# Kernel tuning notes

Measured on AMD Instinct MI355X. Metric: run time of the kernel, lower is better.

The kernel has to match this reference:

```python
import jax, jax.numpy as jnp
import numpy as np

N = 16384   # flat token count
D = 256     # d_model
M = 64      # median_size (attention in_features / hidden_features)
OUT = 1     # output_size


def setup_inputs() -> dict:
    key = jax.random.key(0)
    ks = jax.random.split(key, 12)
    sD = 1.0 / np.sqrt(D)
    sM = 1.0 / np.sqrt(M)
    rn = lambda k, shape, s: (jax.random.normal(k, shape, jnp.float32) * s)
    return {
        "x":    rn(ks[0], (N, D), 1.0),
        "W1":   rn(ks[1], (D, M), sD), "b1": jnp.zeros((M,), jnp.float32),
        # 3 stacked attention blocks
        "Wq":   rn(ks[2], (3, M, M), sM), "bq": jnp.zeros((3, M), jnp.float32),
        "Wk":   rn(ks[3], (3, M, M), sM), "bk": jnp.zeros((3, M), jnp.float32),
        "Wv":   rn(ks[4], (3, M, M), sM), "bv": jnp.zeros((3, M), jnp.float32),
        "Wf1":  rn(ks[5], (3, M, M), sM), "bf1": jnp.zeros((3, M), jnp.float32),
        "Wf2":  rn(ks[6], (3, M, M), sM), "bf2": jnp.zeros((3, M), jnp.float32),
        "ln_g": jnp.ones((3, M), jnp.float32), "ln_b": jnp.zeros((3, M), jnp.float32),
        "Wout": rn(ks[7], (M, OUT), sM), "bout": jnp.zeros((OUT,), jnp.float32),
    }


def leaky(x, slope):
    return jnp.where(x >= 0, x, slope * x)


def layer_norm(x, g, b, eps=1e-5):
    mu = jnp.mean(x, axis=-1, keepdims=True)
    var = jnp.mean((x - mu) ** 2, axis=-1, keepdims=True)
    return (x - mu) * jax.lax.rsqrt(var + eps) * g + b


def attn_block(x, Wq, bq, Wk, bk, Wv, bv, Wf1, bf1, Wf2, bf2):
    # per-token outer-product attention: attn[n] = softmax(q[n] k[n]^T) over last dim
    q = x @ Wq + bq            # [N, M]
    k = x @ Wk + bk
    v = x @ Wv + bv
    a = jax.nn.softmax(q[:, :, None] * k[:, None, :], axis=-1)   # [N, M, M]
    y = jnp.einsum('nij,nj->ni', a, v) + x                       # residual add (x += x0)
    h = leaky(y @ Wf1 + bf1, 0.01)                               # LeakyReLU(0.01)
    h = h @ Wf2 + bf2
    return h + y                                                 # pred=False residual


def reference(x, W1, b1, Wq, bq, Wk, bk, Wv, bv, Wf1, bf1, Wf2, bf2, ln_g, ln_b, Wout, bout):
    h = x @ W1 + b1                 # Linear_1
    res = leaky(h, 0.1)             # x1 = LeakyReLU(0.1)(h)
    cur = h                         # transformer_1 is applied to pre-activation h
    for t in range(3):
        a = attn_block(cur, Wq[t], bq[t], Wk[t], bk[t], Wv[t], bv[t],
                       Wf1[t], bf1[t], Wf2[t], bf2[t])
        a = layer_norm(a, ln_g[t], ln_b[t])
        res = a + res               # x2 = LN(...) + x1, etc.
        cur = res
    out = leaky(res @ Wout + bout, 0.1).reshape(-1, OUT)
    return (out, out, out, out, out)
```

## Files before the change

kernel.cpp:

```cpp
#include <hip/hip_runtime.h>

#define NTOK 16384
#define TB 16

typedef float f32x4_t __attribute__((ext_vector_type(4)));
typedef short s16x8_t __attribute__((ext_vector_type(8)));

union bfpack { unsigned int u[4]; s16x8_t v; };

__device__ __forceinline__ unsigned int pk2bf(float lo, float hi) {
    unsigned int r;
    asm("v_cvt_pk_bf16_f32 %0, %1, %2" : "=v"(r) : "v"(lo), "v"(hi));
    return r;
}
__device__ __forceinline__ unsigned short f2bf(float f) {
    unsigned int r;
    asm("v_cvt_pk_bf16_f32 %0, %1, %1" : "=v"(r) : "v"(f));
    return (unsigned short)r;
}
__device__ __forceinline__ unsigned short f2bf_host_style(float f) {
    unsigned int x = __float_as_uint(f);
    x += 0x7fffu + ((x >> 16) & 1u);
    return (unsigned short)(x >> 16);
}
__device__ __forceinline__ float fexp2(float x) {
#if __has_builtin(__builtin_amdgcn_exp2f)
    return __builtin_amdgcn_exp2f(x);
#else
    return exp2f(x);
#endif
}
__device__ __forceinline__ float frcp(float x) {
#if __has_builtin(__builtin_amdgcn_rcpf)
    return __builtin_amdgcn_rcpf(x);
#else
    return 1.0f / x;
#endif
}
__device__ __forceinline__ float frsq(float x) {
#if __has_builtin(__builtin_amdgcn_rsqf)
    return __builtin_amdgcn_rsqf(x);
#else
    return rsqrtf(x);
#endif
}

__global__ __launch_bounds__(256)
void prep_kernel(const float* __restrict__ W1,
                 const float* __restrict__ Wq, const float* __restrict__ Wk,
                 const float* __restrict__ Wv, const float* __restrict__ Wf1,
                 const float* __restrict__ Wf2, unsigned short* __restrict__ wsb)
{
    const int i = blockIdx.x * 256 + threadIdx.x;
    if (i < 16384) {
        const int m = i >> 8, k = i & 255;
        wsb[i] = f2bf_host_style(W1[k * 64 + m]);
    } else if (i < 77824) {
        const int u  = i - 16384;
        const int mi = u >> 12;
        const int st = mi / 5, q = mi % 5;
        const int r  = u & 4095;
        const int hk = r >> 11;
        const int r1 = r & 2047;
        const int w  = r1 >> 9;
        const int r2 = r1 & 511;
        const int l  = r2 >> 3;
        const int e  = r2 & 7;
        const int m  = w * 16 + (l & 15);
        const int k  = hk * 32 + (l >> 4) * 8 + e;
        const float* src = q == 0 ? Wq : q == 1 ? Wk : q == 2 ? Wv : q == 3 ? Wf1 : Wf2;
        wsb[i] = f2bf_host_style(src[st * 4096 + k * 64 + m]);
    }
}

__global__ __launch_bounds__(256, 4)
void tf3_kernel(const float* __restrict__ x,
                const float* __restrict__ b1,
                const float* __restrict__ bq, const float* __restrict__ bk,
                const float* __restrict__ bv,
                const float* __restrict__ bf1, const float* __restrict__ bf2,
                const float* __restrict__ lng, const float* __restrict__ lnb,
                const float* __restrict__ Wout, const float* __restrict__ bout,
                const unsigned short* __restrict__ wsb,
                float* __restrict__ out)
{
    __shared__ __align__(16) char smem[15104];
    unsigned short* a_lds = (unsigned short*)smem;
    float* q_lds  = (float*)(smem + 2048);
    float* ky_lds = (float*)(smem + 6400);
    float* v_lds  = (float*)(smem + 10752);
    char*  x_img  = smem + 2048;

    const int tid = threadIdx.x;
    const int wv  = tid >> 6;
    const int l   = tid & 63;
    const int n0  = blockIdx.x * TB;

    const int lr  = l & 15;
    const int q4  = l >> 4;
    const int c   = wv * 16 + lr;

    const int ge = lr;
    const int tg = wv * 4 + q4;

    float res_reg[4], cur_reg[4];

    auto LOADM = [&](int mat, s16x8_t& r0, s16x8_t& r1) {
        const char* gb = (const char*)(wsb + 16384 + mat * 4096) + wv * 1024 + l * 16;
        r0 = *reinterpret_cast<const s16x8_t*>(gb);
        r1 = *reinterpret_cast<const s16x8_t*>(gb + 4096);
    };
    auto mmd = [&](s16x8_t af0, s16x8_t af1, s16x8_t b0, s16x8_t b1) -> f32x4_t {
        f32x4_t acc = __builtin_amdgcn_mfma_f32_16x16x32_bf16(af0, b0, (f32x4_t){0.f,0.f,0.f,0.f}, 0, 0, 0);
        acc = __builtin_amdgcn_mfma_f32_16x16x32_bf16(af1, b1, acc, 0, 0, 0);
        return acc;
    };

    s16x8_t bq0, bq1, bk0, bk1, bv0, bv1;
    s16x8_t f10, f11, f20, f21;

    LOADM(0, bq0, bq1); LOADM(1, bk0, bk1); LOADM(2, bv0, bv1);

    {
        const int r  = tid & 15;
        const int cb = tid >> 4;
        const float* xp = x + (size_t)(n0 + r) * 256 + cb * 16;
        const float4 u0 = *reinterpret_cast<const float4*>(xp);
        const float4 u1 = *reinterpret_cast<const float4*>(xp + 4);
        const float4 u2 = *reinterpret_cast<const float4*>(xp + 8);
        const float4 u3 = *reinterpret_cast<const float4*>(xp + 12);
        bfpack P0, P1;
        P0.u[0] = pk2bf(u0.x, u0.y); P0.u[1] = pk2bf(u0.z, u0.w);
        P0.u[2] = pk2bf(u1.x, u1.y); P0.u[3] = pk2bf(u1.z, u1.w);
        P1.u[0] = pk2bf(u2.x, u2.y); P1.u[1] = pk2bf(u2.z, u2.w);
        P1.u[2] = pk2bf(u3.x, u3.y); P1.u[3] = pk2bf(u3.z, u3.w);
        char* rowb = x_img + r * 512;
        *reinterpret_cast<s16x8_t*>(rowb + (((cb * 2    ) ^ (r & 7)) << 4)) = P0.v;
        *reinterpret_cast<s16x8_t*>(rowb + (((cb * 2 + 1) ^ (r & 7)) << 4)) = P1.v;
    }
    __syncthreads();

    f32x4_t acch = {0.f, 0.f, 0.f, 0.f};
    #pragma unroll
    for (int s5 = 0; s5 < 8; ++s5) {
        const s16x8_t af = *reinterpret_cast<const s16x8_t*>(
            x_img + lr * 512 + (((s5 * 4 + q4) ^ (lr & 7)) << 4));
        const s16x8_t bf = *reinterpret_cast<const s16x8_t*>(&wsb[c * 256 + s5 * 32 + q4 * 8]);
        acch = __builtin_amdgcn_mfma_f32_16x16x32_bf16(af, bf, acch, 0, 0, 0);
    }
    __syncthreads();
    {
        const float bb = b1[c];
        #pragma unroll
        for (int rg = 0; rg < 4; ++rg)
            q_lds[(q4 * 4 + rg) * 68 + c] = acch[rg] + bb;
    }
    __syncthreads();
    #pragma unroll
    for (int tt = 0; tt < 4; ++tt) {
        const int t = wv * 4 + tt;
        const float h = q_lds[t * 68 + l];
        cur_reg[tt] = h;
        res_reg[tt] = h >= 0.f ? h : 0.1f * h;
        a_lds[t * 64 + (((l >> 3) ^ (t & 7)) * 8) + (l & 7)] = f2bf(h);
    }

    for (int st = 0; st < 3; ++st) {
        const float bqv  = bq[st * 64 + c];
        const float bkv  = bk[st * 64 + c];
        const float bvv  = bv[st * 64 + c];
        const float bf1v = bf1[st * 64 + c];
        const float bf2v = bf2[st * 64 + c];
        const float lngv = lng[st * 64 + l];
        const float lnbv = lnb[st * 64 + l];

        __syncthreads();
        {
            const s16x8_t af0 = *reinterpret_cast<const s16x8_t*>(&a_lds[lr * 64 + ((q4       ^ (lr & 7)) * 8)]);
            const s16x8_t af1 = *reinterpret_cast<const s16x8_t*>(&a_lds[lr * 64 + (((4 + q4) ^ (lr & 7)) * 8)]);
            f32x4_t aq = mmd(af0, af1, bq0, bq1);
            f32x4_t ak = mmd(af0, af1, bk0, bk1);
            f32x4_t av = mmd(af0, af1, bv0, bv1);
            #pragma unroll
            for (int rg = 0; rg < 4; ++rg) {
                const int tr = q4 * 4 + rg;
                q_lds[tr * 68 + c]  = aq[rg] + bqv;
                ky_lds[tr * 68 + c] = ak[rg] + bkv;
                v_lds[tr * 68 + c]  = av[rg] + bvv;
            }
        }
        LOADM(st * 5 + 3, f10, f11);
        __syncthreads();

        float kmax_t[4], kmin_t[4];
        {
            const float4 kv = *reinterpret_cast<const float4*>(&ky_lds[tg * 68 + ge * 4]);
            float kmx = fmaxf(fmaxf(kv.x, kv.y), fmaxf(kv.z, kv.w));
            float kmn = fminf(fminf(kv.x, kv.y), fminf(kv.z, kv.w));
            #pragma unroll
            for (int m = 1; m < 16; m <<= 1) {
                kmx = fmaxf(kmx, __shfl_xor(kmx, m, 64));
                kmn = fminf(kmn, __shfl_xor(kmn, m, 64));
            }
            #pragma unroll
            for (int tt = 0; tt < 4; ++tt) {
                kmax_t[tt] = __shfl(kmx, tt * 16, 64);
                kmin_t[tt] = __shfl(kmn, tt * 16, 64);
            }
        }
        #pragma unroll
        for (int tt = 0; tt < 4; ++tt) {
            const int t = wv * 4 + tt;
            const float qs = q_lds[t * 68 + l] * 1.44269504088896340736f;
            const float m2 = fmaxf(qs * kmax_t[tt], qs * kmin_t[tt]);
            const float* kb = &ky_lds[t * 68];
            const float* vb = &v_lds[t * 68];
            float4 ka0 = *reinterpret_cast<const float4*>(kb);
            float4 ka1 = *reinterpret_cast<const float4*>(kb + 4);
            float4 va0 = *reinterpret_cast<const float4*>(vb);
            float4 va1 = *reinterpret_cast<const float4*>(vb + 4);
            float s0 = 0.f, s1 = 0.f, p0 = 0.f, p1 = 0.f;
            #pragma unroll
            for (int j = 0; j < 64; j += 8) {
                float4 kn0, kn1, vn0, vn1;
                if (j < 56) {
                    kn0 = *reinterpret_cast<const float4*>(kb + j + 8);
                    kn1 = *reinterpret_cast<const float4*>(kb + j + 12);
                    vn0 = *reinterpret_cast<const float4*>(vb + j + 8);
                    vn1 = *reinterpret_cast<const float4*>(vb + j + 12);
                }
                const float e0 = fexp2(fmaf(qs, ka0.x, -m2)); s0 += e0; p0 = fmaf(e0, va0.x, p0);
                const float e1 = fexp2(fmaf(qs, ka0.y, -m2)); s1 += e1; p1 = fmaf(e1, va0.y, p1);
                const float e2 = fexp2(fmaf(qs, ka0.z, -m2)); s0 += e2; p0 = fmaf(e2, va0.z, p0);
                const float e3 = fexp2(fmaf(qs, ka0.w, -m2)); s1 += e3; p1 = fmaf(e3, va0.w, p1);
                const float e4 = fexp2(fmaf(qs, ka1.x, -m2)); s0 += e4; p0 = fmaf(e4, va1.x, p0);
                const float e5 = fexp2(fmaf(qs, ka1.y, -m2)); s1 += e5; p1 = fmaf(e5, va1.y, p1);
                const float e6 = fexp2(fmaf(qs, ka1.z, -m2)); s0 += e6; p0 = fmaf(e6, va1.z, p0);
                const float e7 = fexp2(fmaf(qs, ka1.w, -m2)); s1 += e7; p1 = fmaf(e7, va1.w, p1);
                ka0 = kn0; ka1 = kn1; va0 = vn0; va1 = vn1;
            }
            const float y = (p0 + p1) * frcp(s0 + s1) + cur_reg[tt];
            ky_lds[t * 68 + l] = y;
        }
        LOADM(st * 5 + 4, f20, f21);
        __syncthreads();

        {
            f32x4_t acc = {0.f, 0.f, 0.f, 0.f};
            #pragma unroll
            for (int kh = 0; kh < 2; ++kh) {
                const float* yp = &ky_lds[lr * 68 + kh * 32 + q4 * 8];
                const float4 y0 = *reinterpret_cast<const float4*>(yp);
                const float4 y1 = *reinterpret_cast<const float4*>(yp + 4);
                bfpack P;
                P.u[0] = pk2bf(y0.x, y0.y); P.u[1] = pk2bf(y0.z, y0.w);
                P.u[2] = pk2bf(y1.x, y1.y); P.u[3] = pk2bf(y1.z, y1.w);
                acc = __builtin_amdgcn_mfma_f32_16x16x32_bf16(P.v, kh ? f11 : f10, acc, 0, 0, 0);
            }
            #pragma unroll
            for (int rg = 0; rg < 4; ++rg) {
                const int tr = q4 * 4 + rg;
                float h = acc[rg] + bf1v;
                h = h >= 0.f ? h : 0.01f * h;
                a_lds[tr * 64 + (((c >> 3) ^ (tr & 7)) * 8) + (c & 7)] = f2bf(h);
            }
        }
        if (st < 2) {
            LOADM((st + 1) * 5 + 0, bq0, bq1);
            LOADM((st + 1) * 5 + 1, bk0, bk1);
        }
        __syncthreads();

        {
            const s16x8_t ag0 = *reinterpret_cast<const s16x8_t*>(&a_lds[lr * 64 + ((q4       ^ (lr & 7)) * 8)]);
            const s16x8_t ag1 = *reinterpret_cast<const s16x8_t*>(&a_lds[lr * 64 + (((4 + q4) ^ (lr & 7)) * 8)]);
            f32x4_t acc = mmd(ag0, ag1, f20, f21);
            #pragma unroll
            for (int rg = 0; rg < 4; ++rg) {
                const int tr = q4 * 4 + rg;
                ky_lds[tr * 68 + c] += acc[rg] + bf2v;
            }
        }
        if (st < 2) LOADM((st + 1) * 5 + 2, bv0, bv1);
        __syncthreads();

        {
            const float4 av4 = *reinterpret_cast<const float4*>(&ky_lds[tg * 68 + ge * 4]);
            float ssum = av4.x + av4.y + av4.z + av4.w;
            #pragma unroll
            for (int m = 1; m < 16; m <<= 1) ssum += __shfl_xor(ssum, m, 64);
            const float mug = ssum * 0.015625f;
            const float d0 = av4.x - mug, d1 = av4.y - mug, d2 = av4.z - mug, d3 = av4.w - mug;
            float vsum = d0 * d0 + d1 * d1 + d2 * d2 + d3 * d3;
            #pragma unroll
            for (int m = 1; m < 16; m <<= 1) vsum += __shfl_xor(vsum, m, 64);
            #pragma unroll
            for (int tt = 0; tt < 4; ++tt) {
                const int t = wv * 4 + tt;
                const float mu = __shfl(mug, tt * 16, 64);
                const float vv = __shfl(vsum, tt * 16, 64);
                const float rs = frsq(vv * 0.015625f + 1e-5f);
                const float a  = ky_lds[t * 68 + l];
                const float an = (a - mu) * rs * lngv + lnbv;
                const float rnew = res_reg[tt] + an;
                res_reg[tt] = rnew;
                cur_reg[tt] = rnew;
                a_lds[t * 64 + (((l >> 3) ^ (t & 7)) * 8) + (l & 7)] = f2bf(rnew);
            }
        }
    }

    const float wo = Wout[l];
    const float bo = bout[0];
    #pragma unroll
    for (int tt = 0; tt < 4; ++tt)
        q_lds[(wv * 4 + tt) * 68 + l] = res_reg[tt] * wo;
    {
        const float4 pv = *reinterpret_cast<const float4*>(&q_lds[tg * 68 + ge * 4]);
        float p = pv.x + pv.y + pv.z + pv.w;
        #pragma unroll
        for (int m = 1; m < 16; m <<= 1) p += __shfl_xor(p, m, 64);
        if (ge == 0) {
            float o = p + bo;
            o = o >= 0.f ? o : 0.1f * o;
            #pragma unroll
            for (int c5 = 0; c5 < 5; ++c5)
                out[(size_t)c5 * NTOK + n0 + tg] = o;
        }
    }
}

extern "C" void kernel_launch(void* const* d_in, const int* in_sizes, int n_in,
                              void* d_out, int out_size, void* d_ws, size_t ws_size,
                              hipStream_t stream) {
    const float* x    = (const float*)d_in[0];
    const float* W1   = (const float*)d_in[1];
    const float* b1   = (const float*)d_in[2];
    const float* Wq   = (const float*)d_in[3];
    const float* bq   = (const float*)d_in[4];
    const float* Wk   = (const float*)d_in[5];
    const float* bk   = (const float*)d_in[6];
    const float* Wv   = (const float*)d_in[7];
    const float* bv   = (const float*)d_in[8];
    const float* Wf1  = (const float*)d_in[9];
    const float* bf1  = (const float*)d_in[10];
    const float* Wf2  = (const float*)d_in[11];
    const float* bf2  = (const float*)d_in[12];
    const float* lngp = (const float*)d_in[13];
    const float* lnbp = (const float*)d_in[14];
    const float* Wout = (const float*)d_in[15];
    const float* bout = (const float*)d_in[16];
    float* outp = (float*)d_out;
    unsigned short* wsb = (unsigned short*)d_ws;

    hipLaunchKernelGGL(prep_kernel, dim3(304), dim3(256), 0, stream,
                       W1, Wq, Wk, Wv, Wf1, Wf2, wsb);
    hipLaunchKernelGGL(tf3_kernel, dim3(NTOK / TB), dim3(256), 0, stream,
                       x, b1, bq, bk, bv, bf1, bf2, lngp, lnbp, Wout, bout,
                       (const unsigned short*)wsb, outp);
}
```

Measured before the change: 54.54 us.

## Make each wave own four tokens independently and drop block-wide barriers

Each wavefront now processes its own 4 tokens end to end, with a private LDS region, so all __syncthreads barriers between GEMM, softmax and layernorm stages go away. Every GEMM now computes all 64 output columns per wave as four MFMA tiles, with only 4 of the 16 A rows meaningful. That wastes three quarters of the MFMA work, and weights are reloaded from global or L2 on every use instead of being held in registers. The softmax inner loop also loses its software prefetch.

```diff
diff --git a/kernel.cpp b/kernel.cpp
--- a/kernel.cpp
+++ b/kernel.cpp
@@ -1,7 +1,6 @@
 #include <hip/hip_runtime.h>
 
 #define NTOK 16384
-#define TB 16
 
 typedef float f32x4_t __attribute__((ext_vector_type(4)));
 typedef short s16x8_t __attribute__((ext_vector_type(8)));
@@ -84,117 +83,131 @@
                 const unsigned short* __restrict__ wsb,
                 float* __restrict__ out)
 {
-    __shared__ __align__(16) char smem[15104];
-    unsigned short* a_lds = (unsigned short*)smem;
-    float* q_lds  = (float*)(smem + 2048);
-    float* ky_lds = (float*)(smem + 6400);
-    float* v_lds  = (float*)(smem + 10752);
-    char*  x_img  = smem + 2048;
+    __shared__ __align__(16) char smem[4 * 3840];
 
     const int tid = threadIdx.x;
     const int wv  = tid >> 6;
     const int l   = tid & 63;
-    const int n0  = blockIdx.x * TB;
-
     const int lr  = l & 15;
     const int q4  = l >> 4;
-    const int c   = wv * 16 + lr;
-
-    const int ge = lr;
-    const int tg = wv * 4 + q4;
+    const int tw0 = blockIdx.x * 16 + wv * 4;
+
+    char* wbase = smem + wv * 3840;
+    unsigned short* a_w = (unsigned short*)wbase;
+    float* q_w  = (float*)(wbase + 576);
+    float* ky_w = (float*)(wbase + 1664);
+    float* v_w  = (float*)(wbase + 2752);
+    char*  x_img = wbase + 576;
 
     float res_reg[4], cur_reg[4];
 
-    auto LOADM = [&](int mat, s16x8_t& r0, s16x8_t& r1) {
-        const char* gb = (const char*)(wsb + 16384 + mat * 4096) + wv * 1024 + l * 16;
-        r0 = *reinterpret_cast<const s16x8_t*>(gb);
-        r1 = *reinterpret_cast<const s16x8_t*>(gb + 4096);
+    auto LDB4 = [&](int mat, int kh, s16x8_t b[4]) {
+        const char* gb = (const char*)(wsb + 16384) + mat * 8192 + kh * 4096 + l * 16;
+        b[0] = *reinterpret_cast<const s16x8_t*>(gb);
+        b[1] = *reinterpret_cast<const s16x8_t*>(gb + 1024);
+        b[2] = *reinterpret_cast<const s16x8_t*>(gb + 2048);
+        b[3] = *reinterpret_cast<const s16x8_t*>(gb + 3072);
     };
-    auto mmd = [&](s16x8_t af0, s16x8_t af1, s16x8_t b0, s16x8_t b1) -> f32x4_t {
-        f32x4_t acc = __builtin_amdgcn_mfma_f32_16x16x32_bf16(af0, b0, (f32x4_t){0.f,0.f,0.f,0.f}, 0, 0, 0);
-        acc = __builtin_amdgcn_mfma_f32_16x16x32_bf16(af1, b1, acc, 0, 0, 0);
-        return acc;
+    auto GEMM_A = [&](int mat, f32x4_t acc[4]) {
+        #pragma unroll
+        for (int kh = 0; kh < 2; ++kh) {
+            const s16x8_t af = *reinterpret_cast<const s16x8_t*>(
+                (char*)a_w + (lr & 3) * 144 + (kh * 4 + q4) * 16);
+            s16x8_t b[4];
+            LDB4(mat, kh, b);
+            #pragma unroll
+            for (int tile = 0; tile < 4; ++tile)
+                acc[tile] = __builtin_amdgcn_mfma_f32_16x16x32_bf16(af, b[tile], acc[tile], 0, 0, 0);
+        }
     };
 
-    s16x8_t bq0, bq1, bk0, bk1, bv0, bv1;
-    s16x8_t f10, f11, f20, f21;
-
-    LOADM(0, bq0, bq1); LOADM(1, bk0, bk1); LOADM(2, bv0, bv1);
-
     {
-        const int r  = tid & 15;
-        const int cb = tid >> 4;
-        const float* xp = x + (size_t)(n0 + r) * 256 + cb * 16;
-        const float4 u0 = *reinterpret_cast<const float4*>(xp);
-        const float4 u1 = *reinterpret_cast<const float4*>(xp + 4);
-        const float4 u2 = *reinterpret_cast<const float4*>(xp + 8);
-        const float4 u3 = *reinterpret_cast<const float4*>(xp + 12);
-        bfpack P0, P1;
-        P0.u[0] = pk2bf(u0.x, u0.y); P0.u[1] = pk2bf(u0.z, u0.w);
-        P0.u[2] = pk2bf(u1.x, u1.y); P0.u[3] = pk2bf(u1.z, u1.w);
-        P1.u[0] = pk2bf(u2.x, u2.y); P1.u[1] = pk2bf(u2.z, u2.w);
-        P1.u[2] = pk2bf(u3.x, u3.y); P1.u[3] = pk2bf(u3.z, u3.w);
-        char* rowb = x_img + r * 512;
-        *reinterpret_cast<s16x8_t*>(rowb + (((cb * 2    ) ^ (r & 7)) << 4)) = P0.v;
-        *reinterpret_cast<s16x8_t*>(rowb + (((cb * 2 + 1) ^ (r & 7)) << 4)) = P1.v;
-    }
-    __syncthreads();
-
-    f32x4_t acch = {0.f, 0.f, 0.f, 0.f};
-    #pragma unroll
-    for (int s5 = 0; s5 < 8; ++s5) {
-        const s16x8_t af = *reinterpret_cast<const s16x8_t*>(
-            x_img + lr * 512 + (((s5 * 4 + q4) ^ (lr & 7)) << 4));
-        const s16x8_t bf = *reinterpret_cast<const s16x8_t*>(&wsb[c * 256 + s5 * 32 + q4 * 8]);
-        acch = __builtin_amdgcn_mfma_f32_16x16x32_bf16(af, bf, acch, 0, 0, 0);
-    }
-    __syncthreads();
+        const int xr = l >> 4, xc = l & 15;
+        const float* xrow = x + (size_t)(tw0 + xr) * 256;
+        #pragma unroll
+        for (int i = 0; i < 4; ++i) {
+            const float4 u = *reinterpret_cast<const float4*>(xrow + xc * 4 + i * 64);
+            uint2 p;
+            p.x = pk2bf(u.x, u.y);
+            p.y = pk2bf(u.z, u.w);
+            *reinterpret_cast<uint2*>(x_img + xr * 528 + xc * 8 + i * 128) = p;
+        }
+    }
     {
-        const float bb = b1[c];
-        #pragma unroll
-        for (int rg = 0; rg < 4; ++rg)
-            q_lds[(q4 * 4 + rg) * 68 + c] = acch[rg] + bb;
-    }
-    __syncthreads();
+        f32x4_t acc[4] = {{0,0,0,0},{0,0,0,0},{0,0,0,0},{0,0,0,0}};
+        #pragma unroll
+        for (int s5 = 0; s5 < 8; ++s5) {
+            const s16x8_t af = *reinterpret_cast<const s16x8_t*>(
+                x_img + (lr & 3) * 528 + s5 * 64 + q4 * 16);
+            #pragma unroll
+            for (int tile = 0; tile < 4; ++tile) {
+                const s16x8_t bf = *reinterpret_cast<const s16x8_t*>(
+                    (const char*)wsb + (size_t)(tile * 16 + lr) * 512 + s5 * 64 + q4 * 16);
+                acc[tile] = __builtin_amdgcn_mfma_f32_16x16x32_bf16(af, bf, acc[tile], 0, 0, 0);
+            }
+        }
+        if (q4 == 0) {
+            #pragma unroll
+            for (int tile = 0; tile < 4; ++tile) {
+                const float bb = b1[tile * 16 + lr];
+                #pragma unroll
+                for (int rg = 0; rg < 4; ++rg)
+                    q_w[rg * 68 + tile * 16 + lr] = acc[tile][rg] + bb;
+            }
+        }
+    }
     #pragma unroll
     for (int tt = 0; tt < 4; ++tt) {
-        const int t = wv * 4 + tt;
-        const float h = q_lds[t * 68 + l];
+        const float h = q_w[tt * 68 + l];
         cur_reg[tt] = h;
         res_reg[tt] = h >= 0.f ? h : 0.1f * h;
-        a_lds[t * 64 + (((l >> 3) ^ (t & 7)) * 8) + (l & 7)] = f2bf(h);
+        a_w[tt * 72 + l] = f2bf(h);
     }
 
     for (int st = 0; st < 3; ++st) {
-        const float bqv  = bq[st * 64 + c];
-        const float bkv  = bk[st * 64 + c];
-        const float bvv  = bv[st * 64 + c];
-        const float bf1v = bf1[st * 64 + c];
-        const float bf2v = bf2[st * 64 + c];
-        const float lngv = lng[st * 64 + l];
-        const float lnbv = lnb[st * 64 + l];
-
-        __syncthreads();
-        {
-            const s16x8_t af0 = *reinterpret_cast<const s16x8_t*>(&a_lds[lr * 64 + ((q4       ^ (lr & 7)) * 8)]);
-            const s16x8_t af1 = *reinterpret_cast<const s16x8_t*>(&a_lds[lr * 64 + (((4 + q4) ^ (lr & 7)) * 8)]);
-            f32x4_t aq = mmd(af0, af1, bq0, bq1);
-            f32x4_t ak = mmd(af0, af1, bk0, bk1);
-            f32x4_t av = mmd(af0, af1, bv0, bv1);
-            #pragma unroll
-            for (int rg = 0; rg < 4; ++rg) {
-                const int tr = q4 * 4 + rg;
-                q_lds[tr * 68 + c]  = aq[rg] + bqv;
-                ky_lds[tr * 68 + c] = ak[rg] + bkv;
-                v_lds[tr * 68 + c]  = av[rg] + bvv;
-            }
-        }
-        LOADM(st * 5 + 3, f10, f11);
-        __syncthreads();
+        {
+            f32x4_t aq[4] = {{0,0,0,0},{0,0,0,0},{0,0,0,0},{0,0,0,0}};
+            GEMM_A(st * 5 + 0, aq);
+            if (q4 == 0) {
+                #pragma unroll
+                for (int tile = 0; tile < 4; ++tile) {
+                    const float bb = bq[st * 64 + tile * 16 + lr];
+                    #pragma unroll
+                    for (int rg = 0; rg < 4; ++rg)
+                        q_w[rg * 68 + tile * 16 + lr] = aq[tile][rg] + bb;
+                }
+            }
+        }
+        {
+            f32x4_t ak[4] = {{0,0,0,0},{0,0,0,0},{0,0,0,0},{0,0,0,0}};
+            GEMM_A(st * 5 + 1, ak);
+            if (q4 == 0) {
+                #pragma unroll
+                for (int tile = 0; tile < 4; ++tile) {
+                    const float bb = bk[st * 64 + tile * 16 + lr];
+                    #pragma unroll
+                    for (int rg = 0; rg < 4; ++rg)
+                        ky_w[rg * 68 + tile * 16 + lr] = ak[tile][rg] + bb;
+                }
+            }
+        }
+        {
+            f32x4_t av[4] = {{0,0,0,0},{0,0,0,0},{0,0,0,0},{0,0,0,0}};
+            GEMM_A(st * 5 + 2, av);
+            if (q4 == 0) {
+                #pragma unroll
+                for (int tile = 0; tile < 4; ++tile) {
+                    const float bb = bv[st * 64 + tile * 16 + lr];
+                    #pragma unroll
+                    for (int rg = 0; rg < 4; ++rg)
+                        v_w[rg * 68 + tile * 16 + lr] = av[tile][rg] + bb;
+                }
+            }
+        }
 
         float kmax_t[4], kmin_t[4];
         {
-            const float4 kv = *reinterpret_cast<const float4*>(&ky_lds[tg * 68 + ge * 4]);
+            const float4 kv = *reinterpret_cast<const float4*>(ky_w + q4 * 68 + lr * 4);
             float kmx = fmaxf(fmaxf(kv.x, kv.y), fmaxf(kv.z, kv.w));
             float kmn = fminf(fminf(kv.x, kv.y), fminf(kv.z, kv.w));
             #pragma unroll
@@ -210,82 +223,70 @@
         }
         #pragma unroll
         for (int tt = 0; tt < 4; ++tt) {
-            const int t = wv * 4 + tt;
-            const float qs = q_lds[t * 68 + l] * 1.44269504088896340736f;
+            const float qs = q_w[tt * 68 + l] * 1.44269504088896340736f;
             const float m2 = fmaxf(qs * kmax_t[tt], qs * kmin_t[tt]);
-            const float* kb = &ky_lds[t * 68];
-            const float* vb = &v_lds[t * 68];
-            float4 ka0 = *reinterpret_cast<const float4*>(kb);
-            float4 ka1 = *reinterpret_cast<const float4*>(kb + 4);
-            float4 va0 = *reinterpret_cast<const float4*>(vb);
-            float4 va1 = *reinterpret_cast<const float4*>(vb + 4);
+            const float* kb = ky_w + tt * 68;
+            const float* vb = v_w + tt * 68;
             float s0 = 0.f, s1 = 0.f, p0 = 0.f, p1 = 0.f;
             #pragma unroll
-            for (int j = 0; j < 64; j += 8) {
-                float4 kn0, kn1, vn0, vn1;
-                if (j < 56) {
-                    kn0 = *reinterpret_cast<const float4*>(kb + j + 8);
-                    kn1 = *reinterpret_cast<const float4*>(kb + j + 12);
-                    vn0 = *reinterpret_cast<const float4*>(vb + j + 8);
-                    vn1 = *reinterpret_cast<const float4*>(vb + j + 12);
-                }
-                const float e0 = fexp2(fmaf(qs, ka0.x, -m2)); s0 += e0; p0 = fmaf(e0, va0.x, p0);
-                const float e1 = fexp2(fmaf(qs, ka0.y, -m2)); s1 += e1; p1 = fmaf(e1, va0.y, p1);
-                const float e2 = fexp2(fmaf(qs, ka0.z, -m2)); s0 += e2; p0 = fmaf(e2, va0.z, p0);
-                const float e3 = fexp2(fmaf(qs, ka0.w, -m2)); s1 += e3; p1 = fmaf(e3, va0.w, p1);
-                const float e4 = fexp2(fmaf(qs, ka1.x, -m2)); s0 += e4; p0 = fmaf(e4, va1.x, p0);
-                const float e5 = fexp2(fmaf(qs, ka1.y, -m2)); s1 += e5; p1 = fmaf(e5, va1.y, p1);
-                const float e6 = fexp2(fmaf(qs, ka1.z, -m2)); s0 += e6; p0 = fmaf(e6, va1.z, p0);
-                const float e7 = fexp2(fmaf(qs, ka1.w, -m2)); s1 += e7; p1 = fmaf(e7, va1.w, p1);
-                ka0 = kn0; ka1 = kn1; va0 = vn0; va1 = vn1;
+            for (int j = 0; j < 64; j += 4) {
+                const float4 kj = *reinterpret_cast<const float4*>(kb + j);
+                const float4 vj = *reinterpret_cast<const float4*>(vb + j);
+                const float e0 = fexp2(fmaf(qs, kj.x, -m2)); s0 += e0; p0 = fmaf(e0, vj.x, p0);
+                const float e1 = fexp2(fmaf(qs, kj.y, -m2)); s1 += e1; p1 = fmaf(e1, vj.y, p1);
+                const float e2 = fexp2(fmaf(qs, kj.z, -m2)); s0 += e2; p0 = fmaf(e2, vj.z, p0);
+                const float e3 = fexp2(fmaf(qs, kj.w, -m2)); s1 += e3; p1 = fmaf(e3, vj.w, p1);
             }
             const float y = (p0 + p1) * frcp(s0 + s1) + cur_reg[tt];
-            ky_lds[t * 68 + l] = y;
-        }
-        LOADM(st * 5 + 4, f20, f21);
-        __syncthreads();
-
-        {
-            f32x4_t acc = {0.f, 0.f, 0.f, 0.f};
+            ky_w[tt * 68 + l] = y;
+        }
+
+        {
+            f32x4_t acc[4] = {{0,0,0,0},{0,0,0,0},{0,0,0,0},{0,0,0,0}};
             #pragma unroll
             for (int kh = 0; kh < 2; ++kh) {
-                const float* yp = &ky_lds[lr * 68 + kh * 32 + q4 * 8];
+                const float* yp = ky_w + (lr & 3) * 68 + kh * 32 + q4 * 8;
                 const float4 y0 = *reinterpret_cast<const float4*>(yp);
                 const float4 y1 = *reinterpret_cast<const float4*>(yp + 4);
                 bfpack P;
                 P.u[0] = pk2bf(y0.x, y0.y); P.u[1] = pk2bf(y0.z, y0.w);
                 P.u[2] = pk2bf(y1.x, y1.y); P.u[3] = pk2bf(y1.z, y1.w);
-                acc = __builtin_amdgcn_mfma_f32_16x16x32_bf16(P.v, kh ? f11 : f10, acc, 0, 0, 0);
-            }
-            #pragma unroll
-            for (int rg = 0; rg < 4; ++rg) {
-                const int tr = q4 * 4 + rg;
-                float h = acc[rg] + bf1v;
-                h = h >= 0.f ? h : 0.01f * h;
-                a_lds[tr * 64 + (((c >> 3) ^ (tr & 7)) * 8) + (c & 7)] = f2bf(h);
-            }
-        }
-        if (st < 2) {
-            LOADM((st + 1) * 5 + 0, bq0, bq1);
-            LOADM((st + 1) * 5 + 1, bk0, bk1);
-        }
-        __syncthreads();
-
-        {
-            const s16x8_t ag0 = *reinterpret_cast<const s16x8_t*>(&a_lds[lr * 64 + ((q4       ^ (lr & 7)) * 8)]);
-            const s16x8_t ag1 = *reinterpret_cast<const s16x8_t*>(&a_lds[lr * 64 + (((4 + q4) ^ (lr & 7)) * 8)]);
-            f32x4_t acc = mmd(ag0, ag1, f20, f21);
-            #pragma unroll
-            for (int rg = 0; rg < 4; ++rg) {
-                const int tr = q4 * 4 + rg;
-                ky_lds[tr * 68 + c] += acc[rg] + bf2v;
-            }
-        }
-        if (st < 2) LOADM((st + 1) * 5 + 2, bv0, bv1);
-        __syncthreads();
-
-        {
-            const float4 av4 = *reinterpret_cast<const float4*>(&ky_lds[tg * 68 + ge * 4]);
+                s16x8_t b[4];
+                LDB4(st * 5 + 3, kh, b);
+                #pragma unroll
+                for (int tile = 0; tile < 4; ++tile)
+                    acc[tile] = __builtin_amdgcn_mfma_f32_16x16x32_bf16(P.v, b[tile], acc[tile], 0, 0, 0);
+            }
+            if (q4 == 0) {
+                #pragma unroll
+                for (int tile = 0; tile < 4; ++tile) {
+                    const float bb = bf1[st * 64 + tile * 16 + lr];
+                    #pragma unroll
+                    for (int rg = 0; rg < 4; ++rg) {
+                        float h = acc[tile][rg] + bb;
+                        h = h >= 0.f ? h : 0.01f * h;
+                        a_w[rg * 72 + tile * 16 + lr] = f2bf(h);
+                    }
+                }
+            }
+        }
+
+        {
+            f32x4_t acc[4] = {{0,0,0,0},{0,0,0,0},{0,0,0,0},{0,0,0,0}};
+            GEMM_A(st * 5 + 4, acc);
+            if (q4 == 0) {
+                #pragma unroll
+                for (int tile = 0; tile < 4; ++tile) {
+                    const float bb = bf2[st * 64 + tile * 16 + lr];
+                    #pragma unroll
+                    for (int rg = 0; rg < 4; ++rg)
+                        ky_w[rg * 68 + tile * 16 + lr] += acc[tile][rg] + bb;
+                }
+            }
+        }
+
+        {
+            const float4 av4 = *reinterpret_cast<const float4*>(ky_w + q4 * 68 + lr * 4);
             float ssum = av4.x + av4.y + av4.z + av4.w;
             #pragma unroll
             for (int m = 1; m < 16; m <<= 1) ssum += __shfl_xor(ssum, m, 64);
@@ -294,38 +295,40 @@
             float vsum = d0 * d0 + d1 * d1 + d2 * d2 + d3 * d3;
             #pragma unroll
             for (int m = 1; m < 16; m <<= 1) vsum += __shfl_xor(vsum, m, 64);
+            const float lngv = lng[st * 64 + l];
+            const float lnbv = lnb[st * 64 + l];
             #pragma unroll
             for (int tt = 0; tt < 4; ++tt) {
-                const int t = wv * 4 + tt;
                 const float mu = __shfl(mug, tt * 16, 64);
                 const float vv = __shfl(vsum, tt * 16, 64);
                 const float rs = frsq(vv * 0.015625f + 1e-5f);
-                const float a  = ky_lds[t * 68 + l];
+                const float a  = ky_w[tt * 68 + l];
                 const float an = (a - mu) * rs * lngv + lnbv;
                 const float rnew = res_reg[tt] + an;
                 res_reg[tt] = rnew;
                 cur_reg[tt] = rnew;
-                a_lds[t * 64 + (((l >> 3) ^ (t & 7)) * 8) + (l & 7)] = f2bf(rnew);
-            }
-        }
-    }
-
-    const float wo = Wout[l];
-    const float bo = bout[0];
-    #pragma unroll
-    for (int tt = 0; tt < 4; ++tt)
-        q_lds[(wv * 4 + tt) * 68 + l] = res_reg[tt] * wo;
+                a_w[tt * 72 + l] = f2bf(rnew);
+            }
+        }
+    }
+
     {
-        const float4 pv = *reinterpret_cast<const float4*>(&q_lds[tg * 68 + ge * 4]);
+        const float wo = Wout[l];
+        const float bo = bout[0];
+        #pragma unroll
+        for (int tt = 0; tt < 4; ++tt)
+            q_w[tt * 68 + l] = res_reg[tt] * wo;
+        const float4 pv = *reinterpret_cast<const float4*>(q_w + q4 * 68 + lr * 4);
         float p = pv.x + pv.y + pv.z + pv.w;
         #pragma unroll
         for (int m = 1; m < 16; m <<= 1) p += __shfl_xor(p, m, 64);
-        if (ge == 0) {
+        if (lr == 0) {
             float o = p + bo;
             o = o >= 0.f ? o : 0.1f * o;
+            const int token = tw0 + q4;
             #pragma unroll
             for (int c5 = 0; c5 < 5; ++c5)
-                out[(size_t)c5 * NTOK + n0 + tg] = o;
+                out[(size_t)c5 * NTOK + token] = o;
         }
     }
 }
@@ -355,7 +358,7 @@
 
     hipLaunchKernelGGL(prep_kernel, dim3(304), dim3(256), 0, stream,
                        W1, Wq, Wk, Wv, Wf1, Wf2, wsb);
-    hipLaunchKernelGGL(tf3_kernel, dim3(NTOK / TB), dim3(256), 0, stream,
+    hipLaunchKernelGGL(tf3_kernel, dim3(NTOK / 16), dim3(256), 0, stream,
                        x, b1, bq, bk, bv, bf1, bf2, lngp, lnbp, Wout, bout,
                        (const unsigned short*)wsb, outp);
 }
```

Measured after the change: 69.28 us. 27.0% more time.

## Halve tokens per block to 8 with two waves covering 32 columns each

Applied to the files above, without the earlier changes.

The token tile drops from 16 to 8 and the block from four waves to two. Each wave now produces 32 output columns using paired 16x16 MFMAs, which doubles the number of blocks and raises the per-wave MFMA count. The MFMA tiles still span 16 rows, so half of each tile's rows hold stale LDS data and the total matrix work effectively doubles. Weight prefetches are also regrouped: the next stage's q/k/v fragments now load together after the FFN instead of being spread across the stage, and the softmax inner loop loses its explicit software prefetch.

```diff
diff --git a/kernel.cpp b/kernel.cpp
--- a/kernel.cpp
+++ b/kernel.cpp
@@ -1,7 +1,7 @@
 #include <hip/hip_runtime.h>
 
 #define NTOK 16384
-#define TB 16
+#define TB 8
 
 typedef float f32x4_t __attribute__((ext_vector_type(4)));
 typedef short s16x8_t __attribute__((ext_vector_type(8)));
@@ -73,7 +73,7 @@
     }
 }
 
-__global__ __launch_bounds__(256, 4)
+__global__ __launch_bounds__(128, 4)
 void tf3_kernel(const float* __restrict__ x,
                 const float* __restrict__ b1,
                 const float* __restrict__ bq, const float* __restrict__ bk,
@@ -98,32 +98,32 @@
 
     const int lr  = l & 15;
     const int q4  = l >> 4;
-    const int c   = wv * 16 + lr;
-
-    const int ge = lr;
-    const int tg = wv * 4 + q4;
+    const int c0  = wv * 32 + lr;
+    const int c1  = c0 + 16;
 
     float res_reg[4], cur_reg[4];
 
-    auto LOADM = [&](int mat, s16x8_t& r0, s16x8_t& r1) {
-        const char* gb = (const char*)(wsb + 16384 + mat * 4096) + wv * 1024 + l * 16;
-        r0 = *reinterpret_cast<const s16x8_t*>(gb);
-        r1 = *reinterpret_cast<const s16x8_t*>(gb + 4096);
+    auto LOADM2 = [&](int mat, s16x8_t& a00, s16x8_t& a01, s16x8_t& a10, s16x8_t& a11) {
+        const char* gb = (const char*)(wsb + 16384) + mat * 8192 + (wv * 2) * 1024 + l * 16;
+        a00 = *reinterpret_cast<const s16x8_t*>(gb);
+        a10 = *reinterpret_cast<const s16x8_t*>(gb + 1024);
+        a01 = *reinterpret_cast<const s16x8_t*>(gb + 4096);
+        a11 = *reinterpret_cast<const s16x8_t*>(gb + 4096 + 1024);
     };
-    auto mmd = [&](s16x8_t af0, s16x8_t af1, s16x8_t b0, s16x8_t b1) -> f32x4_t {
-        f32x4_t acc = __builtin_amdgcn_mfma_f32_16x16x32_bf16(af0, b0, (f32x4_t){0.f,0.f,0.f,0.f}, 0, 0, 0);
-        acc = __builtin_amdgcn_mfma_f32_16x16x32_bf16(af1, b1, acc, 0, 0, 0);
-        return acc;
-    };
-
-    s16x8_t bq0, bq1, bk0, bk1, bv0, bv1;
-    s16x8_t f10, f11, f20, f21;
-
-    LOADM(0, bq0, bq1); LOADM(1, bk0, bk1); LOADM(2, bv0, bv1);
+
+    s16x8_t bq00, bq01, bq10, bq11;
+    s16x8_t bk00, bk01, bk10, bk11;
+    s16x8_t bv00, bv01, bv10, bv11;
+    s16x8_t f100, f101, f110, f111;
+    s16x8_t f200, f201, f210, f211;
+
+    LOADM2(0, bq00, bq01, bq10, bq11);
+    LOADM2(1, bk00, bk01, bk10, bk11);
+    LOADM2(2, bv00, bv01, bv10, bv11);
 
     {
-        const int r  = tid & 15;
-        const int cb = tid >> 4;
+        const int r  = tid >> 4;
+        const int cb = tid & 15;
         const float* xp = x + (size_t)(n0 + r) * 256 + cb * 16;
         const float4 u0 = *reinterpret_cast<const float4*>(xp);
         const float4 u1 = *reinterpret_cast<const float4*>(xp + 4);
@@ -140,20 +140,27 @@
     }
     __syncthreads();
 
-    f32x4_t acch = {0.f, 0.f, 0.f, 0.f};
+    f32x4_t acch0 = {0.f, 0.f, 0.f, 0.f};
+    f32x4_t acch1 = {0.f, 0.f, 0.f, 0.f};
     #pragma unroll
     for (int s5 = 0; s5 < 8; ++s5) {
         const s16x8_t af = *reinterpret_cast<const s16x8_t*>(
             x_img + lr * 512 + (((s5 * 4 + q4) ^ (lr & 7)) << 4));
-        const s16x8_t bf = *reinterpret_cast<const s16x8_t*>(&wsb[c * 256 + s5 * 32 + q4 * 8]);
-        acch = __builtin_amdgcn_mfma_f32_16x16x32_bf16(af, bf, acch, 0, 0, 0);
+        const s16x8_t bf0 = *reinterpret_cast<const s16x8_t*>(&wsb[c0 * 256 + s5 * 32 + q4 * 8]);
+        const s16x8_t bf1f = *reinterpret_cast<const s16x8_t*>(&wsb[c1 * 256 + s5 * 32 + q4 * 8]);
+        acch0 = __builtin_amdgcn_mfma_f32_16x16x32_bf16(af, bf0, acch0, 0, 0, 0);
+        acch1 = __builtin_amdgcn_mfma_f32_16x16x32_bf16(af, bf1f, acch1, 0, 0, 0);
     }
     __syncthreads();
     {
-        const float bb = b1[c];
+        const float bb0 = b1[c0];
+        const float bb1 = b1[c1];
         #pragma unroll
-        for (int rg = 0; rg < 4; ++rg)
-            q_lds[(q4 * 4 + rg) * 68 + c] = acch[rg] + bb;
+        for (int rg = 0; rg < 4; ++rg) {
+            const int tr = q4 * 4 + rg;
+            q_lds[tr * 68 + c0] = acch0[rg] + bb0;
+            q_lds[tr * 68 + c1] = acch1[rg] + bb1;
+        }
     }
     __syncthreads();
     #pragma unroll
@@ -166,11 +173,11 @@
     }
 
     for (int st = 0; st < 3; ++st) {
-        const float bqv  = bq[st * 64 + c];
-        const float bkv  = bk[st * 64 + c];
-        const float bvv  = bv[st * 64 + c];
-        const float bf1v = bf1[st * 64 + c];
-        const float bf2v = bf2[st * 64 + c];
+        const float bqv0 = bq[st * 64 + c0], bqv1 = bq[st * 64 + c1];
+        const float bkv0 = bk[st * 64 + c0], bkv1 = bk[st * 64 + c1];
+        const float bvv0 = bv[st * 64 + c0], bvv1 = bv[st * 64 + c1];
+        const float bf1v0 = bf1[st * 64 + c0], bf1v1 = bf1[st * 64 + c1];
+        const float bf2v0 = bf2[st * 64 + c0], bf2v1 = bf2[st * 64 + c1];
         const float lngv = lng[st * 64 + l];
         const float lnbv = lnb[st * 64 + l];
 
@@ -178,23 +185,36 @@
         {
             const s16x8_t af0 = *reinterpret_cast<const s16x8_t*>(&a_lds[lr * 64 + ((q4       ^ (lr & 7)) * 8)]);
             const s16x8_t af1 = *reinterpret_cast<const s16x8_t*>(&a_lds[lr * 64 + (((4 + q4) ^ (lr & 7)) * 8)]);
-            f32x4_t aq = mmd(af0, af1, bq0, bq1);
-            f32x4_t ak = mmd(af0, af1, bk0, bk1);
-            f32x4_t av = mmd(af0, af1, bv0, bv1);
+            f32x4_t aq0 = __builtin_amdgcn_mfma_f32_16x16x32_bf16(af0, bq00, (f32x4_t){0.f,0.f,0.f,0.f}, 0, 0, 0);
+            aq0 = __builtin_amdgcn_mfma_f32_16x16x32_bf16(af1, bq01, aq0, 0, 0, 0);
+            f32x4_t aq1 = __builtin_amdgcn_mfma_f32_16x16x32_bf16(af0, bq10, (f32x4_t){0.f,0.f,0.f,0.f}, 0, 0, 0);
+            aq1 = __builtin_amdgcn_mfma_f32_16x16x32_bf16(af1, bq11, aq1, 0, 0, 0);
+            f32x4_t ak0 = __builtin_amdgcn_mfma_f32_16x16x32_bf16(af0, bk00, (f32x4_t){0.f,0.f,0.f,0.f}, 0, 0, 0);
+            ak0 = __builtin_amdgcn_mfma_f32_16x16x32_bf16(af1, bk01, ak0, 0, 0, 0);
+            f32x4_t ak1 = __builtin_amdgcn_mfma_f32_16x16x32_bf16(af0, bk10, (f32x4_t){0.f,0.f,0.f,0.f}, 0, 0, 0);
+            ak1 = __builtin_amdgcn_mfma_f32_16x16x32_bf16(af1, bk11, ak1, 0, 0, 0);
+            f32x4_t av0 = __builtin_amdgcn_mfma_f32_16x16x32_bf16(af0, bv00, (f32x4_t){0.f,0.f,0.f,0.f}, 0, 0, 0);
+            av0 = __builtin_amdgcn_mfma_f32_16x16x32_bf16(af1, bv01, av0, 0, 0, 0);
+            f32x4_t av1 = __builtin_amdgcn_mfma_f32_16x16x32_bf16(af0, bv10, (f32x4_t){0.f,0.f,0.f,0.f}, 0, 0, 0);
+            av1 = __builtin_amdgcn_mfma_f32_16x16x32_bf16(af1, bv11, av1, 0, 0, 0);
             #pragma unroll
             for (int rg = 0; rg < 4; ++rg) {
                 const int tr = q4 * 4 + rg;
-                q_lds[tr * 68 + c]  = aq[rg] + bqv;
-                ky_lds[tr * 68 + c] = ak[rg] + bkv;
-                v_lds[tr * 68 + c]  = av[rg] + bvv;
-            }
-        }
-        LOADM(st * 5 + 3, f10, f11);
+                q_lds[tr * 68 + c0]  = aq0[rg] + bqv0;
+                q_lds[tr * 68 + c1]  = aq1[rg] + bqv1;
+                ky_lds[tr * 68 + c0] = ak0[rg] + bkv0;
+                ky_lds[tr * 68 + c1] = ak1[rg] + bkv1;
+                v_lds[tr * 68 + c0]  = av0[rg] + bvv0;
+                v_lds[tr * 68 + c1]  = av1[rg] + bvv1;
+            }
+        }
+        LOADM2(st * 5 + 3, f100, f101, f110, f111);
         __syncthreads();
 
         float kmax_t[4], kmin_t[4];
         {
-            const float4 kv = *reinterpret_cast<const float4*>(&ky_lds[tg * 68 + ge * 4]);
+            const int tg = wv * 4 + q4;
+            const float4 kv = *reinterpret_cast<const float4*>(&ky_lds[tg * 68 + lr * 4]);
             float kmx = fmaxf(fmaxf(kv.x, kv.y), fmaxf(kv.z, kv.w));
             float kmn = fminf(fminf(kv.x, kv.y), fminf(kv.z, kv.w));
             #pragma unroll
@@ -215,38 +235,24 @@
             const float m2 = fmaxf(qs * kmax_t[tt], qs * kmin_t[tt]);
             const float* kb = &ky_lds[t * 68];
             const float* vb = &v_lds[t * 68];
-            float4 ka0 = *reinterpret_cast<const float4*>(kb);
-            float4 ka1 = *reinterpret_cast<const float4*>(kb + 4);
-            float4 va0 = *reinterpret_cast<const float4*>(vb);
-            float4 va1 = *reinterpret_cast<const float4*>(vb + 4);
             float s0 = 0.f, s1 = 0.f, p0 = 0.f, p1 = 0.f;
             #pragma unroll
-            for (int j = 0; j < 64; j += 8) {
-                float4 kn0, kn1, vn0, vn1;
-                if (j < 56) {
-                    kn0 = *reinterpret_cast<const float4*>(kb + j + 8);
-                    kn1 = *reinterpret_cast<const float4*>(kb + j + 12);
-                    vn0 = *reinterpret_cast<const float4*>(vb + j + 8);
-                    vn1 = *reinterpret_cast<const float4*>(vb + j + 12);
-                }
-                const float e0 = fexp2(fmaf(qs, ka0.x, -m2)); s0 += e0; p0 = fmaf(e0, va0.x, p0);
-                const float e1 = fexp2(fmaf(qs, ka0.y, -m2)); s1 += e1; p1 = fmaf(e1, va0.y, p1);
-                const float e2 = fexp2(fmaf(qs, ka0.z, -m2)); s0 += e2; p0 = fmaf(e2, va0.z, p0);
-                const float e3 = fexp2(fmaf(qs, ka0.w, -m2)); s1 += e3; p1 = fmaf(e3, va0.w, p1);
-                const float e4 = fexp2(fmaf(qs, ka1.x, -m2)); s0 += e4; p0 = fmaf(e4, va1.x, p0);
-                const float e5 = fexp2(fmaf(qs, ka1.y, -m2)); s1 += e5; p1 = fmaf(e5, va1.y, p1);
-                const float e6 = fexp2(fmaf(qs, ka1.z, -m2)); s0 += e6; p0 = fmaf(e6, va1.z, p0);
-                const float e7 = fexp2(fmaf(qs, ka1.w, -m2)); s1 += e7; p1 = fmaf(e7, va1.w, p1);
-                ka0 = kn0; ka1 = kn1; va0 = vn0; va1 = vn1;
+            for (int j = 0; j < 64; j += 4) {
+                const float4 kj = *reinterpret_cast<const float4*>(kb + j);
+                const float4 vj = *reinterpret_cast<const float4*>(vb + j);
+                const float e0 = fexp2(fmaf(qs, kj.x, -m2)); s0 += e0; p0 = fmaf(e0, vj.x, p0);
+                const float e1 = fexp2(fmaf(qs, kj.y, -m2)); s1 += e1; p1 = fmaf(e1, vj.y, p1);
+                const float e2v = fexp2(fmaf(qs, kj.z, -m2)); s0 += e2v; p0 = fmaf(e2v, vj.z, p0);
+                const float e3 = fexp2(fmaf(qs, kj.w, -m2)); s1 += e3; p1 = fmaf(e3, vj.w, p1);
             }
             const float y = (p0 + p1) * frcp(s0 + s1) + cur_reg[tt];
             ky_lds[t * 68 + l] = y;
         }
-        LOADM(st * 5 + 4, f20, f21);
-        __syncthreads();
-
-        {
-            f32x4_t acc = {0.f, 0.f, 0.f, 0.f};
+        LOADM2(st * 5 + 4, f200, f201, f210, f211);
+        __syncthreads();
+
+        {
+            f32x4_t a0 = {0.f,0.f,0.f,0.f}, a1 = {0.f,0.f,0.f,0.f};
             #pragma unroll
             for (int kh = 0; kh < 2; ++kh) {
                 const float* yp = &ky_lds[lr * 68 + kh * 32 + q4 * 8];
@@ -255,37 +261,45 @@
                 bfpack P;
                 P.u[0] = pk2bf(y0.x, y0.y); P.u[1] = pk2bf(y0.z, y0.w);
                 P.u[2] = pk2bf(y1.x, y1.y); P.u[3] = pk2bf(y1.z, y1.w);
-                acc = __builtin_amdgcn_mfma_f32_16x16x32_bf16(P.v, kh ? f11 : f10, acc, 0, 0, 0);
+                a0 = __builtin_amdgcn_mfma_f32_16x16x32_bf16(P.v, kh ? f101 : f100, a0, 0, 0, 0);
+                a1 = __builtin_amdgcn_mfma_f32_16x16x32_bf16(P.v, kh ? f111 : f110, a1, 0, 0, 0);
             }
             #pragma unroll
             for (int rg = 0; rg < 4; ++rg) {
                 const int tr = q4 * 4 + rg;
-                float h = acc[rg] + bf1v;
-                h = h >= 0.f ? h : 0.01f * h;
-                a_lds[tr * 64 + (((c >> 3) ^ (tr & 7)) * 8) + (c & 7)] = f2bf(h);
-            }
-        }
-        if (st < 2) {
-            LOADM((st + 1) * 5 + 0, bq0, bq1);
-            LOADM((st + 1) * 5 + 1, bk0, bk1);
+                float h0 = a0[rg] + bf1v0; h0 = h0 >= 0.f ? h0 : 0.01f * h0;
+                float h1 = a1[rg] + bf1v1; h1 = h1 >= 0.f ? h1 : 0.01f * h1;
+                a_lds[tr * 64 + (((c0 >> 3) ^ (tr & 7)) * 8) + (c0 & 7)] = f2bf(h0);
+                a_lds[tr * 64 + (((c1 >> 3) ^ (tr & 7)) * 8) + (c1 & 7)] = f2bf(h1);
+            }
         }
         __syncthreads();
 
         {
             const s16x8_t ag0 = *reinterpret_cast<const s16x8_t*>(&a_lds[lr * 64 + ((q4       ^ (lr & 7)) * 8)]);
             const s16x8_t ag1 = *reinterpret_cast<const s16x8_t*>(&a_lds[lr * 64 + (((4 + q4) ^ (lr & 7)) * 8)]);
-            f32x4_t acc = mmd(ag0, ag1, f20, f21);
+            f32x4_t a0 = __builtin_amdgcn_mfma_f32_16x16x32_bf16(ag0, f200, (f32x4_t){0.f,0.f,0.f,0.f}, 0, 0, 0);
+            a0 = __builtin_amdgcn_mfma_f32_16x16x32_bf16(ag1, f201, a0, 0, 0, 0);
+            f32x4_t a1 = __builtin_amdgcn_mfma_f32_16x16x32_bf16(ag0, f210, (f32x4_t){0.f,0.f,0.f,0.f}, 0, 0, 0);
+            a1 = __builtin_amdgcn_mfma_f32_16x16x32_bf16(ag1, f211, a1, 0, 0, 0);
             #pragma unroll
             for (int rg = 0; rg < 4; ++rg) {
                 const int tr = q4 * 4 + rg;
-                ky_lds[tr * 68 + c] += acc[rg] + bf2v;
-            }
-        }
-        if (st < 2) LOADM((st + 1) * 5 + 2, bv0, bv1);
-        __syncthreads();
-
-        {
-            const float4 av4 = *reinterpret_cast<const float4*>(&ky_lds[tg * 68 + ge * 4]);
+                ky_lds[tr * 68 + c0] += a0[rg] + bf2v0;
+                ky_lds[tr * 68 + c1] += a1[rg] + bf2v1;
+            }
+        }
+        __syncthreads();
+
+        if (st < 2) {
+            LOADM2((st + 1) * 5 + 0, bq00, bq01, bq10, bq11);
+            LOADM2((st + 1) * 5 + 1, bk00, bk01, bk10, bk11);
+            LOADM2((st + 1) * 5 + 2, bv00, bv01, bv10, bv11);
+        }
+
+        {
+            const int tg = wv * 4 + q4;
+            const float4 av4 = *reinterpret_cast<const float4*>(&ky_lds[tg * 68 + lr * 4]);
             float ssum = av4.x + av4.y + av4.z + av4.w;
             #pragma unroll
             for (int m = 1; m < 16; m <<= 1) ssum += __shfl_xor(ssum, m, 64);
@@ -316,11 +330,12 @@
     for (int tt = 0; tt < 4; ++tt)
         q_lds[(wv * 4 + tt) * 68 + l] = res_reg[tt] * wo;
     {
-        const float4 pv = *reinterpret_cast<const float4*>(&q_lds[tg * 68 + ge * 4]);
+        const int tg = wv * 4 + q4;
+        const float4 pv = *reinterpret_cast<const float4*>(&q_lds[tg * 68 + lr * 4]);
         float p = pv.x + pv.y + pv.z + pv.w;
         #pragma unroll
         for (int m = 1; m < 16; m <<= 1) p += __shfl_xor(p, m, 64);
-        if (ge == 0) {
+        if (lr == 0) {
             float o = p + bo;
             o = o >= 0.f ? o : 0.1f * o;
             #pragma unroll
@@ -355,7 +370,7 @@
 
     hipLaunchKernelGGL(prep_kernel, dim3(304), dim3(256), 0, stream,
                        W1, Wq, Wk, Wv, Wf1, Wf2, wsb);
-    hipLaunchKernelGGL(tf3_kernel, dim3(NTOK / TB), dim3(256), 0, stream,
+    hipLaunchKernelGGL(tf3_kernel, dim3(NTOK / TB), dim3(128), 0, stream,
                        x, b1, bq, bk, bv, bf1, bf2, lngp, lnbp, Wout, bout,
                        (const unsigned short*)wsb, outp);
 }
```

Result: slower. 78.38 us (+43.7%).
